# Kernel tuning notes

Hardware: AMD Instinct MI355X
Metric: run time of the kernel (lower is better)

## Reference

```python
import math
import jax, jax.numpy as jnp
import numpy as np

SR = 22050
W_STEP = 256
W = 2048
TAU_MAX = 2048
MIDI_START = 5
MIDI_END = 85
OCT = 12.0


def _lag_constants():
    # midi -> lag (eq. 4): lag = sr / (440 * 2**((m-69)/12))
    midis = np.arange(MIDI_START, MIDI_END)
    f = 440.0 * np.power(2.0, (midis - 69) / OCT)
    c_ms = SR / f
    return c_ms, np.ceil(c_ms).astype(np.int64), np.floor(c_ms).astype(np.int64)


def setup_inputs() -> dict:
    key = jax.random.key(0)
    x = jax.random.normal(key, (16, 88200), dtype=jnp.float32)
    return {"x": x}


def reference(x):
    B, T = x.shape
    F = (T - W) // W_STEP + 1  # number of frames (unfold with stride w_step)
    idx = jnp.arange(F)[:, None] * W_STEP + jnp.arange(W)[None, :]
    frames = x[:, idx].reshape(B * F, W)  # (BF, W)

    # --- difference function d(tau) via FFT autocorrelation -------------
    x_cumsum = jnp.concatenate(
        [jnp.zeros((B * F, 1), frames.dtype), jnp.cumsum(frames * frames, axis=-1)],
        axis=-1,
    )  # (BF, W+1)
    size = W + TAU_MAX
    p2 = (size // 32).bit_length()
    nice = (16, 18, 20, 24, 25, 27, 30, 32)
    size_pad = min(n * 2 ** p2 for n in nice if n * 2 ** p2 >= size)  # 4096 here
    fc = jnp.fft.rfft(frames, size_pad)
    acf = jnp.fft.irfft(fc * jnp.conj(fc), size_pad)[:, :TAU_MAX]
    df = (
        jnp.flip(x_cumsum[:, W - TAU_MAX + 1 : W + 1], axis=-1)  # x_cumsum[W:W-tau:-1]
        + x_cumsum[:, W : W + 1]
        - x_cumsum[:, :TAU_MAX]
        - 2.0 * acf
    )  # (BF, tau_max)

    # --- cumulative mean normalized difference function (eq. 1/2) -------
    ar = jnp.arange(1, TAU_MAX, dtype=df.dtype)
    cmndf = df[:, 1:] * ar / (jnp.cumsum(df[:, 1:], axis=-1) + 1e-8)
    cmndfs = jnp.concatenate([jnp.ones((B * F, 1), df.dtype), cmndf], axis=-1)

    # --- yingram: linear interpolation at midi lags ----------------------
    c_ms, ceil_i, floor_i = _lag_constants()
    c_ms_j = jnp.asarray(c_ms, dtype=df.dtype)
    denom = jnp.asarray((ceil_i - floor_i), dtype=df.dtype)
    frac = (c_ms_j - jnp.asarray(floor_i, dtype=df.dtype)) / denom
    cf = cmndfs[:, floor_i]
    y = (cmndfs[:, ceil_i] - cf) * frac[None, :] + cf  # (BF, M)

    M = MIDI_END - MIDI_START
    return y.reshape(B, F, M).transpose(0, 2, 1)  # (B, M, F)
```

## Files before the change

kernel.cpp:

```cpp
#include <hip/hip_runtime.h>
#include <math.h>

#define W 2048
#define NB 16
#define TLEN 88200
#define NF 337
#define NMIDI 80

typedef __attribute__((ext_vector_type(8))) short short8;
typedef __attribute__((ext_vector_type(4))) float f32x4;

__device__ __forceinline__ int swix(int t) { return t ^ (((t >> 5) & 7) << 2); }

__device__ __forceinline__ int xoff(int S) {
    int s = S & 7;
    int oct = (S + 256) >> 3;
    return (oct << 6) + (((s + oct) & 7) << 3);
}

__device__ __forceinline__ unsigned int f2bf(float x) {
    unsigned u = __float_as_uint(x);
    u += 0x7FFF + ((u >> 16) & 1);
    return u >> 16;
}

__global__ __launch_bounds__(256) void yin_kernel(const float* __restrict__ x,
                                                  float* __restrict__ out) {
    const int f = blockIdx.x, b = blockIdx.y;
    const int tid = threadIdx.x;
    const int lane = tid & 63, wv = tid >> 6;

    __shared__ unsigned short lds_x[18560];
    __shared__ float cum[2049];
    __shared__ float dfc[2048];
    __shared__ float wsum[4];

    const float* xp = x + (size_t)b * TLEN + (size_t)f * 256;

    float v[16];
    {
        const float4* xq = (const float4*)xp;
        float4 q0 = xq[2 * tid];
        float4 q1 = xq[2 * tid + 1];
        float4 q2 = xq[2 * tid + 2];
        float4 q3 = xq[2 * tid + 3];
        if (tid == 255) {
            q2 = make_float4(0.f, 0.f, 0.f, 0.f);
            q3 = make_float4(0.f, 0.f, 0.f, 0.f);
        }
        v[0]=q0.x; v[1]=q0.y; v[2]=q0.z; v[3]=q0.w;
        v[4]=q1.x; v[5]=q1.y; v[6]=q1.z; v[7]=q1.w;
        v[8]=q2.x; v[9]=q2.y; v[10]=q2.z; v[11]=q2.w;
        v[12]=q3.x; v[13]=q3.y; v[14]=q3.z; v[15]=q3.w;
    }

    float pj[8];
    float etot = 0.f;
    #pragma unroll
    for (int j = 0; j < 8; ++j) { etot = fmaf(v[j], v[j], etot); pj[j] = etot; }

    unsigned D[14];
    #pragma unroll
    for (int i = 0; i < 14; ++i) D[i] = f2bf(v[i]) | (f2bf(v[i + 1]) << 16);
    {
        const int oct = tid + 32;
        #pragma unroll
        for (int s = 0; s < 8; ++s) {
            *(uint4*)(lds_x + (oct << 6) + (((s + oct) & 7) << 3)) =
                make_uint4(D[s], D[s + 2], D[s + 4], D[s + 6]);
        }
    }
    {
        int po = tid >> 3, s = tid & 7;
        *(uint4*)(lds_x + (po << 6) + (((s + po) & 7) << 3)) = make_uint4(0, 0, 0, 0);
        if (tid < 16) {
            int oct2 = 288 + (tid >> 3), s2 = tid & 7;
            *(uint4*)(lds_x + (oct2 << 6) + (((s2 + oct2) & 7) << 3)) = make_uint4(0, 0, 0, 0);
        }
    }

    float inc = etot;
    #pragma unroll
    for (int d = 1; d < 64; d <<= 1) {
        float t = __shfl_up(inc, d, 64);
        if (lane >= d) inc += t;
    }
    if (lane == 63) wsum[wv] = inc;

    __syncthreads();

    {
        float base = inc - etot;
        if (wv > 0) base += wsum[0];
        if (wv > 1) base += wsum[1];
        if (wv > 2) base += wsum[2];
        if (tid == 0) cum[0] = 0.0f;
        #pragma unroll
        for (int j = 0; j < 8; ++j) cum[swix(8 * tid + 1 + j)] = base + pj[j];
    }

    const int L = lane & 15;
    const int q8 = (lane >> 4) << 3;
    const int bA = wv, bB = 7 - wv;
    const int KA = 64 - 8 * wv, KB = 8 + 8 * wv;

    f32x4 accA = {0.f, 0.f, 0.f, 0.f};
    f32x4 accB = {0.f, 0.f, 0.f, 0.f};

    int oA0 = xoff(q8 - 16 * L);
    int oA1 = xoff(q8 - 16 * L + 32);
    int oP0 = xoff(q8 + L + 256 * bA);
    int oP1 = xoff(q8 + L + 256 * bA + 32);
    int oR0 = xoff(q8 + L + 256 * bB);
    int oR1 = xoff(q8 + L + 256 * bB + 32);

    int kc = 0;
    for (; kc < KB; kc += 2) {
        short8 a0 = *(const short8*)(lds_x + oA0);
        short8 p0 = *(const short8*)(lds_x + oP0);
        short8 r0 = *(const short8*)(lds_x + oR0);
        accA = __builtin_amdgcn_mfma_f32_16x16x32_bf16(a0, p0, accA, 0, 0, 0);
        accB = __builtin_amdgcn_mfma_f32_16x16x32_bf16(a0, r0, accB, 0, 0, 0);
        short8 a1 = *(const short8*)(lds_x + oA1);
        short8 p1 = *(const short8*)(lds_x + oP1);
        short8 r1 = *(const short8*)(lds_x + oR1);
        accA = __builtin_amdgcn_mfma_f32_16x16x32_bf16(a1, p1, accA, 0, 0, 0);
        accB = __builtin_amdgcn_mfma_f32_16x16x32_bf16(a1, r1, accB, 0, 0, 0);
        oA0 += 512; oA1 += 512; oP0 += 512; oP1 += 512; oR0 += 512; oR1 += 512;
    }
    for (; kc < KA; kc += 2) {
        short8 a0 = *(const short8*)(lds_x + oA0);
        short8 p0 = *(const short8*)(lds_x + oP0);
        accA = __builtin_amdgcn_mfma_f32_16x16x32_bf16(a0, p0, accA, 0, 0, 0);
        short8 a1 = *(const short8*)(lds_x + oA1);
        short8 p1 = *(const short8*)(lds_x + oP1);
        accA = __builtin_amdgcn_mfma_f32_16x16x32_bf16(a1, p1, accA, 0, 0, 0);
        oA0 += 512; oA1 += 512; oP0 += 512; oP1 += 512;
    }

    __syncthreads();

    {
        const float E = cum[swix(2048)];
        const int rq = (lane >> 4) << 6;
        #pragma unroll
        for (int r = 0; r < 4; ++r) {
            int tau = 256 * bA + rq + (r << 4) + L;
            float df = cum[swix(2048 - tau)] + E - cum[swix(tau)] - 2.0f * accA[r];
            dfc[swix(tau)] = df;
        }
        #pragma unroll
        for (int r = 0; r < 4; ++r) {
            int tau = 256 * bB + rq + (r << 4) + L;
            float df = cum[swix(2048 - tau)] + E - cum[swix(tau)] - 2.0f * accB[r];
            dfc[swix(tau)] = df;
        }
    }

    __syncthreads();

    if (wv == 0) {
        float dfv[32];
        float s = 0.f;
        #pragma unroll
        for (int u = 0; u < 8; ++u) {
            int el = swix((lane << 5) | (u << 2));
            f32x4 qd = *(const f32x4*)(dfc + el);
            #pragma unroll
            for (int e = 0; e < 4; ++e) {
                float dv = qd[e];
                if (lane == 0 && u == 0 && e == 0) dv = 0.f;
                dfv[u * 4 + e] = dv;
                s += dv;
            }
        }
        float inc2 = s;
        #pragma unroll
        for (int d = 1; d < 64; d <<= 1) {
            float t = __shfl_up(inc2, d, 64);
            if (lane >= d) inc2 += t;
        }
        float run = inc2 - s;
        #pragma unroll
        for (int u = 0; u < 8; ++u) {
            f32x4 qo;
            #pragma unroll
            for (int e = 0; e < 4; ++e) {
                int tau = (lane << 5) + (u << 2) + e;
                float dv = dfv[u * 4 + e];
                run += dv;
                float y = (float)tau * dv / (run + 1e-8f);
                if (tau == 0) y = 1.0f;
                qo[e] = y;
            }
            int el = swix((lane << 5) | (u << 2));
            *(f32x4*)(dfc + el) = qo;
        }
    }

    __syncthreads();

    if (tid < NMIDI) {
        int midi = tid + 5;
        double c = 22050.0 / (440.0 * exp2(((double)(midi - 69)) / 12.0));
        int fl = (int)c;
        float frac = (float)(c - (double)fl);
        float cf = dfc[swix(fl)];
        float cc = dfc[swix(fl + 1)];
        out[(size_t)b * (NMIDI * NF) + (size_t)tid * NF + f] = fmaf(cc - cf, frac, cf);
    }
}

extern "C" void kernel_launch(void* const* d_in, const int* in_sizes, int n_in,
                              void* d_out, int out_size, void* d_ws, size_t ws_size,
                              hipStream_t stream) {
    const float* x = (const float*)d_in[0];
    float* out = (float*)d_out;
    dim3 grid(NF, NB);
    yin_kernel<<<grid, 256, 0, stream>>>(x, out);
}
```

Baseline: 116.9 us.

## Restructure autocorrelation MFMA loop with register reuse and parallel CMNDF scan

The MFMA loop is reorganized so each wave handles two adjacent lag blocks and reuses A-fragments from earlier groups held in registers, replacing the separate per-block LDS reads. The LDS swizzle gets a new quad rotation to cut bank conflicts, and the cumsum stores are vectorized. The CMNDF prefix scan now spreads across all four waves with a cross-wave partial-sum exchange instead of running on one wave. Midi lag constants are computed in float rather than double, which could shift floor/frac values slightly near integer boundaries.

```diff
diff --git a/kernel.cpp b/kernel.cpp
--- a/kernel.cpp
+++ b/kernel.cpp
@@ -12,10 +12,13 @@
 
 __device__ __forceinline__ int swix(int t) { return t ^ (((t >> 5) & 7) << 2); }
 
+__device__ __forceinline__ int quadrot(int oct, int s) {
+    return (s + 5 * (oct >> 1) + 4 * (oct & 1)) & 7;
+}
 __device__ __forceinline__ int xoff(int S) {
     int s = S & 7;
     int oct = (S + 256) >> 3;
-    return (oct << 6) + (((s + oct) & 7) << 3);
+    return (oct << 6) + (quadrot(oct, s) << 3);
 }
 
 __device__ __forceinline__ unsigned int f2bf(float x) {
@@ -34,6 +37,7 @@
     __shared__ float cum[2049];
     __shared__ float dfc[2048];
     __shared__ float wsum[4];
+    __shared__ float wdsum[4];
 
     const float* xp = x + (size_t)b * TLEN + (size_t)f * 256;
 
@@ -64,18 +68,19 @@
     for (int i = 0; i < 14; ++i) D[i] = f2bf(v[i]) | (f2bf(v[i + 1]) << 16);
     {
         const int oct = tid + 32;
+        const int base = oct << 6;
         #pragma unroll
         for (int s = 0; s < 8; ++s) {
-            *(uint4*)(lds_x + (oct << 6) + (((s + oct) & 7) << 3)) =
+            *(uint4*)(lds_x + base + (quadrot(oct, s) << 3)) =
                 make_uint4(D[s], D[s + 2], D[s + 4], D[s + 6]);
         }
     }
     {
         int po = tid >> 3, s = tid & 7;
-        *(uint4*)(lds_x + (po << 6) + (((s + po) & 7) << 3)) = make_uint4(0, 0, 0, 0);
+        *(uint4*)(lds_x + (po << 6) + (quadrot(po, s) << 3)) = make_uint4(0, 0, 0, 0);
         if (tid < 16) {
             int oct2 = 288 + (tid >> 3), s2 = tid & 7;
-            *(uint4*)(lds_x + (oct2 << 6) + (((s2 + oct2) & 7) << 3)) = make_uint4(0, 0, 0, 0);
+            *(uint4*)(lds_x + (oct2 << 6) + (quadrot(oct2, s2) << 3)) = make_uint4(0, 0, 0, 0);
         }
     }
 
@@ -94,117 +99,115 @@
         if (wv > 0) base += wsum[0];
         if (wv > 1) base += wsum[1];
         if (wv > 2) base += wsum[2];
-        if (tid == 0) cum[0] = 0.0f;
-        #pragma unroll
-        for (int j = 0; j < 8; ++j) cum[swix(8 * tid + 1 + j)] = base + pj[j];
+        f32x4 q0 = {base, base + pj[0], base + pj[1], base + pj[2]};
+        f32x4 q1 = {base + pj[3], base + pj[4], base + pj[5], base + pj[6]};
+        *(f32x4*)(cum + swix(8 * tid)) = q0;
+        *(f32x4*)(cum + swix(8 * tid + 4)) = q1;
+        if (tid == 255) cum[2048] = base + pj[7];
     }
 
     const int L = lane & 15;
     const int q8 = (lane >> 4) << 3;
-    const int bA = wv, bB = 7 - wv;
-    const int KA = 64 - 8 * wv, KB = 8 + 8 * wv;
+    const int bA = 2 * wv;
+    const int KA4 = 16 - 4 * wv;
+
+    const unsigned short* pA[4];
+    const unsigned short* pB[4];
+    #pragma unroll
+    for (int i = 0; i < 4; ++i) {
+        pA[i] = lds_x + xoff(q8 - 16 * L + 32 * i);
+        pB[i] = lds_x + xoff(q8 + L + 256 * bA + 32 * i);
+    }
 
     f32x4 accA = {0.f, 0.f, 0.f, 0.f};
     f32x4 accB = {0.f, 0.f, 0.f, 0.f};
-
-    int oA0 = xoff(q8 - 16 * L);
-    int oA1 = xoff(q8 - 16 * L + 32);
-    int oP0 = xoff(q8 + L + 256 * bA);
-    int oP1 = xoff(q8 + L + 256 * bA + 32);
-    int oR0 = xoff(q8 + L + 256 * bB);
-    int oR1 = xoff(q8 + L + 256 * bB + 32);
-
-    int kc = 0;
-    for (; kc < KB; kc += 2) {
-        short8 a0 = *(const short8*)(lds_x + oA0);
-        short8 p0 = *(const short8*)(lds_x + oP0);
-        short8 r0 = *(const short8*)(lds_x + oR0);
-        accA = __builtin_amdgcn_mfma_f32_16x16x32_bf16(a0, p0, accA, 0, 0, 0);
-        accB = __builtin_amdgcn_mfma_f32_16x16x32_bf16(a0, r0, accB, 0, 0, 0);
-        short8 a1 = *(const short8*)(lds_x + oA1);
-        short8 p1 = *(const short8*)(lds_x + oP1);
-        short8 r1 = *(const short8*)(lds_x + oR1);
-        accA = __builtin_amdgcn_mfma_f32_16x16x32_bf16(a1, p1, accA, 0, 0, 0);
-        accB = __builtin_amdgcn_mfma_f32_16x16x32_bf16(a1, r1, accB, 0, 0, 0);
-        oA0 += 512; oA1 += 512; oP0 += 512; oP1 += 512; oR0 += 512; oR1 += 512;
-    }
-    for (; kc < KA; kc += 2) {
-        short8 a0 = *(const short8*)(lds_x + oA0);
-        short8 p0 = *(const short8*)(lds_x + oP0);
-        accA = __builtin_amdgcn_mfma_f32_16x16x32_bf16(a0, p0, accA, 0, 0, 0);
-        short8 a1 = *(const short8*)(lds_x + oA1);
-        short8 p1 = *(const short8*)(lds_x + oP1);
-        accA = __builtin_amdgcn_mfma_f32_16x16x32_bf16(a1, p1, accA, 0, 0, 0);
-        oA0 += 512; oA1 += 512; oP0 += 512; oP1 += 512;
-    }
-
-    __syncthreads();
-
-    {
-        const float E = cum[swix(2048)];
-        const int rq = (lane >> 4) << 6;
+    short8 aM2[4], aM1[4], aC[4], bC[4];
+
+    #pragma unroll
+    for (int i = 0; i < 4; ++i) { aM2[i] = *(const short8*)pA[i]; bC[i] = *(const short8*)pB[i]; }
+    #pragma unroll
+    for (int i = 0; i < 4; ++i) accA = __builtin_amdgcn_mfma_f32_16x16x32_bf16(aM2[i], bC[i], accA, 0, 0, 0);
+    #pragma unroll
+    for (int i = 0; i < 4; ++i) { aM1[i] = *(const short8*)(pA[i] + 1024); bC[i] = *(const short8*)(pB[i] + 1024); }
+    #pragma unroll
+    for (int i = 0; i < 4; ++i) accA = __builtin_amdgcn_mfma_f32_16x16x32_bf16(aM1[i], bC[i], accA, 0, 0, 0);
+
+    int go = 2048;
+    for (int g = 2; g < KA4; ++g) {
+        #pragma unroll
+        for (int i = 0; i < 4; ++i) { aC[i] = *(const short8*)(pA[i] + go); bC[i] = *(const short8*)(pB[i] + go); }
+        #pragma unroll
+        for (int i = 0; i < 4; ++i) {
+            accA = __builtin_amdgcn_mfma_f32_16x16x32_bf16(aC[i],  bC[i], accA, 0, 0, 0);
+            accB = __builtin_amdgcn_mfma_f32_16x16x32_bf16(aM2[i], bC[i], accB, 0, 0, 0);
+        }
+        #pragma unroll
+        for (int i = 0; i < 4; ++i) { aM2[i] = aM1[i]; aM1[i] = aC[i]; }
+        go += 1024;
+    }
+
+    __syncthreads();
+
+    {
+        const float E = cum[2048];
+        const int hi64 = (lane >> 4) << 6;
         #pragma unroll
         for (int r = 0; r < 4; ++r) {
-            int tau = 256 * bA + rq + (r << 4) + L;
-            float df = cum[swix(2048 - tau)] + E - cum[swix(tau)] - 2.0f * accA[r];
-            dfc[swix(tau)] = df;
+            int tau = (bA << 8) + hi64 + (r << 4) + L;
+            dfc[swix(tau)] = cum[swix(2048 - tau)] + E - cum[swix(tau)] - 2.0f * accA[r];
         }
         #pragma unroll
         for (int r = 0; r < 4; ++r) {
-            int tau = 256 * bB + rq + (r << 4) + L;
-            float df = cum[swix(2048 - tau)] + E - cum[swix(tau)] - 2.0f * accB[r];
-            dfc[swix(tau)] = df;
-        }
-    }
-
-    __syncthreads();
-
-    if (wv == 0) {
-        float dfv[32];
-        float s = 0.f;
-        #pragma unroll
-        for (int u = 0; u < 8; ++u) {
-            int el = swix((lane << 5) | (u << 2));
-            f32x4 qd = *(const f32x4*)(dfc + el);
-            #pragma unroll
-            for (int e = 0; e < 4; ++e) {
-                float dv = qd[e];
-                if (lane == 0 && u == 0 && e == 0) dv = 0.f;
-                dfv[u * 4 + e] = dv;
-                s += dv;
-            }
-        }
+            int tau = ((bA + 1) << 8) + hi64 + (r << 4) + L;
+            dfc[swix(tau)] = cum[swix(2048 - tau)] + E - cum[swix(tau)] - 2.0f * accB[r];
+        }
+    }
+
+    __syncthreads();
+
+    float dv[8];
+    float excl;
+    {
+        int t0 = (wv << 9) + (lane << 3);
+        f32x4 qa = *(const f32x4*)(dfc + swix(t0));
+        f32x4 qb = *(const f32x4*)(dfc + swix(t0 + 4));
+        dv[0]=qa.x; dv[1]=qa.y; dv[2]=qa.z; dv[3]=qa.w;
+        dv[4]=qb.x; dv[5]=qb.y; dv[6]=qb.z; dv[7]=qb.w;
+        if (t0 == 0) dv[0] = 0.f;
+        float s = dv[0]+dv[1]+dv[2]+dv[3]+dv[4]+dv[5]+dv[6]+dv[7];
         float inc2 = s;
         #pragma unroll
         for (int d = 1; d < 64; d <<= 1) {
-            float t = __shfl_up(inc2, d, 64);
-            if (lane >= d) inc2 += t;
-        }
-        float run = inc2 - s;
-        #pragma unroll
-        for (int u = 0; u < 8; ++u) {
-            f32x4 qo;
-            #pragma unroll
-            for (int e = 0; e < 4; ++e) {
-                int tau = (lane << 5) + (u << 2) + e;
-                float dv = dfv[u * 4 + e];
-                run += dv;
-                float y = (float)tau * dv / (run + 1e-8f);
-                if (tau == 0) y = 1.0f;
-                qo[e] = y;
-            }
-            int el = swix((lane << 5) | (u << 2));
-            *(f32x4*)(dfc + el) = qo;
-        }
-    }
-
+            float tsh = __shfl_up(inc2, d, 64);
+            if (lane >= d) inc2 += tsh;
+        }
+        excl = inc2 - s;
+        if (lane == 63) wdsum[wv] = inc2;
+    }
+    __syncthreads();
+    {
+        int t0 = (wv << 9) + (lane << 3);
+        float run = excl;
+        if (wv > 0) run += wdsum[0];
+        if (wv > 1) run += wdsum[1];
+        if (wv > 2) run += wdsum[2];
+        f32x4 qo0, qo1;
+        #pragma unroll
+        for (int j = 0; j < 8; ++j) {
+            run += dv[j];
+            float y = (float)(t0 + j) * dv[j] / (run + 1e-8f);
+            if (t0 + j == 0) y = 1.0f;
+            if (j < 4) qo0[j] = y; else qo1[j - 4] = y;
+        }
+        *(f32x4*)(dfc + swix(t0)) = qo0;
+        *(f32x4*)(dfc + swix(t0 + 4)) = qo1;
+    }
     __syncthreads();
 
     if (tid < NMIDI) {
-        int midi = tid + 5;
-        double c = 22050.0 / (440.0 * exp2(((double)(midi - 69)) / 12.0));
+        float c = 22050.0f / (440.0f * exp2f((float)(tid + 5 - 69) * (1.0f / 12.0f)));
         int fl = (int)c;
-        float frac = (float)(c - (double)fl);
+        float frac = c - (float)fl;
         float cf = dfc[swix(fl)];
         float cc = dfc[swix(fl + 1)];
         out[(size_t)b * (NMIDI * NF) + (size_t)tid * NF + f] = fmaf(cc - cf, frac, cf);
```

Measured after the change: 103.5 us. 11.5% less time.
